# Kernel optimization log

Hardware: AMD Instinct MI355X
Metric: run time of the kernel (lower is better)

Reference implementation:

```python
import jax, jax.numpy as jnp
import numpy as np

N = 512
D = 400          # per-sample feature dim (lstm_hidden_dim * 2)
H = 400          # hidden dim of F_func (lstm_hidden_dim * 2)


def setup_inputs() -> dict:
    key = jax.random.key(0)
    k1, k2, k3, k4, k5, k6 = jax.random.split(key, 6)
    x_samples = jax.random.normal(k1, (N, D), dtype=jnp.float32)
    y_samples = jax.random.normal(k2, (N, D), dtype=jnp.float32)
    # torch nn.Linear default init: U(-1/sqrt(fan_in), 1/sqrt(fan_in))
    b1_bound = 1.0 / np.sqrt(2 * D)
    b2_bound = 1.0 / np.sqrt(H)
    W1 = jax.random.uniform(k3, (H, 2 * D), minval=-b1_bound, maxval=b1_bound, dtype=jnp.float32)
    b1 = jax.random.uniform(k4, (H,), minval=-b1_bound, maxval=b1_bound, dtype=jnp.float32)
    W2 = jax.random.uniform(k5, (1, H), minval=-b2_bound, maxval=b2_bound, dtype=jnp.float32)
    b2 = jax.random.uniform(k6, (1,), minval=-b2_bound, maxval=b2_bound, dtype=jnp.float32)
    return {"x_samples": x_samples, "y_samples": y_samples,
            "W1": W1, "b1": b1, "W2": W2, "b2": b2}


def reference(x_samples, y_samples, W1, b1, W2, b2):
    n = y_samples.shape[0]
    W1x, W1y = W1[:, :D], W1[:, D:]
    hx = x_samples @ W1x.T          # [N, H], contribution of x
    hy = y_samples @ W1y.T          # [N, H], contribution of y

    def score(h):  # second linear + softplus, squeeze out last dim of 1
        return jax.nn.softplus(h @ W2.T + b2)[..., 0]

    # T0[i] = F(x[i], y[i])
    T0 = score(jax.nn.relu(hx + hy + b1))                      # [N]
    # T1[i, j] = F(x[j], y[i])  (x tiled along dim 0, y along dim 1)
    h_pair = jax.nn.relu(hy[:, None, :] + hx[None, :, :] + b1) # [N, N, H]
    T1 = score(h_pair)                                          # [N, N]

    t0_mean = T0.mean()
    lower_bound = t0_mean - (jax.nn.logsumexp(T1, axis=1).mean() - jnp.log(jnp.float32(n)))
    upper_bound = t0_mean - T1.mean()
    return (lower_bound, upper_bound)
```

## Files before the change

### kernel.cpp

```cpp
#include <hip/hip_runtime.h>
#include <math.h>


#define NSAMP 512
#define DIM 400
#define HID 400

__global__ __launch_bounds__(256) void club_gemm_kernel(
    const float* __restrict__ X, const float* __restrict__ Y,
    const float* __restrict__ W1, const float* __restrict__ b1,
    float* __restrict__ hxT0, float* __restrict__ hxT1,
    float* __restrict__ hyb0, float* __restrict__ hyb1)
{
    __shared__ __align__(16) float Ls[64 * 204];
    const int t    = threadIdx.x;
    const int lane = t & 63;
    const int wave = __builtin_amdgcn_readfirstlane(t >> 6);
    const int b    = blockIdx.x;

    const float* __restrict__ Lbase;
    const float* __restrict__ Sbase;
    int Lstride, Lcol0, Lrow0, Lrowmax, Sstride, Scol0, srow_base;
    int kh, mat;

    if (b < 400) {
        mat = 0; kh = b & 1;
        const int bx = (b >> 1) & 7, by = b >> 4;
        Lbase = X;  Lstride = DIM;     Lcol0 = 0;   Lrow0 = bx * 64; Lrowmax = NSAMP - 1;
        Sbase = W1; Sstride = 2 * DIM; Scol0 = 0;
        srow_base = by * 16 + wave * 4;
    } else {
        mat = 1;
        const int bb = b - 400; kh = bb & 1;
        const int bx = (bb >> 1) & 31, by = bb >> 6;
        Lbase = W1; Lstride = 2 * DIM; Lcol0 = DIM; Lrow0 = by * 64; Lrowmax = HID - 1;
        Sbase = Y;  Sstride = DIM;     Scol0 = 0;
        srow_base = bx * 16 + wave * 4;
    }
    const int kc0 = kh * 200;

    for (int idx = t; idx < 3200; idx += 256) {
        int row = idx / 50, q = idx % 50;
        int r = Lrow0 + row; if (r > Lrowmax) r = Lrowmax;
        float4 v = *(const float4*)(Lbase + (size_t)r * Lstride + Lcol0 + kc0 + 4 * q);
        *(float4*)(Ls + row * 204 + 4 * q) = v;
    }
    __syncthreads();

    float acc[4] = {0.f, 0.f, 0.f, 0.f};
#pragma unroll 2
    for (int k4 = 0; k4 < 50; k4++) {
        float4 xv = *(const float4*)(Ls + lane * 204 + 4 * k4);
#pragma unroll
        for (int c = 0; c < 4; c++) {
            const float* __restrict__ wp =
                Sbase + (size_t)(srow_base + c) * Sstride + Scol0 + kc0 + 4 * k4;
            float4 wv = *(const float4*)wp;
            acc[c] = fmaf(xv.x, wv.x, acc[c]);
            acc[c] = fmaf(xv.y, wv.y, acc[c]);
            acc[c] = fmaf(xv.z, wv.z, acc[c]);
            acc[c] = fmaf(xv.w, wv.w, acc[c]);
        }
    }

    if (mat == 0) {
        float* __restrict__ dst = kh ? hxT1 : hxT0;
#pragma unroll
        for (int c = 0; c < 4; c++)
            dst[(size_t)(srow_base + c) * NSAMP + Lrow0 + lane] = acc[c];
    } else {
        float* __restrict__ dst = kh ? hyb1 : hyb0;
        const int h = Lrow0 + lane;
        if (h < HID) {
            if (kh == 0) {
                float bv = b1[h];
#pragma unroll
                for (int c = 0; c < 4; c++) acc[c] += bv;
            }
#pragma unroll
            for (int c = 0; c < 4; c++)
                dst[(size_t)(srow_base + c) * HID + h] = acc[c];
        }
    }
}

__global__ __launch_bounds__(256) void club_combine_kernel(
    const float4* __restrict__ hxT0, const float4* __restrict__ hxT1,
    const float4* __restrict__ hyb0, const float4* __restrict__ hyb1,
    float4* __restrict__ hxT, float4* __restrict__ hyb)
{
    const int idx = blockIdx.x * 256 + threadIdx.x;
    if (idx < 51200) {
        float4 a = hxT0[idx], b = hxT1[idx];
        hxT[idx] = make_float4(a.x + b.x, a.y + b.y, a.z + b.z, a.w + b.w);
    } else {
        const int k = idx - 51200;
        float4 a = hyb0[k], b = hyb1[k];
        hyb[k] = make_float4(a.x + b.x, a.y + b.y, a.z + b.z, a.w + b.w);
    }
}

__global__ __launch_bounds__(256) void club_pair_kernel(
    const float* __restrict__ hxT, const float* __restrict__ hyb,
    const float* __restrict__ W2, const float* __restrict__ b2,
    double* __restrict__ expsum, double* __restrict__ tsum,
    double* __restrict__ diagT)
{
    const int t    = threadIdx.x;
    const int lane = t & 63;
    const int wave = __builtin_amdgcn_readfirstlane(t >> 6);
    const int jx   = blockIdx.x;
    const int j    = jx * 64 + lane;
    const int i    = blockIdx.y * 4 + wave;

    const float* __restrict__ Bp = hxT + j;
    const float* __restrict__ Ap = hyb + (size_t)i * HID;

    float acc0 = 0.f, acc1 = 0.f;
#pragma unroll 2
    for (int g = 0; g < 50; g++) {
        const int h = 8 * g;
        float bv[8];
#pragma unroll
        for (int u = 0; u < 8; u++)
            bv[u] = Bp[(size_t)(h + u) * NSAMP];
        float4 a0 = *(const float4*)(Ap + h);
        float4 a1 = *(const float4*)(Ap + h + 4);
        float4 w0 = *(const float4*)(W2 + h);
        float4 w1 = *(const float4*)(W2 + h + 4);
        acc0 = fmaf(fmaxf(a0.x + bv[0], 0.f), w0.x, acc0);
        acc1 = fmaf(fmaxf(a0.y + bv[1], 0.f), w0.y, acc1);
        acc0 = fmaf(fmaxf(a0.z + bv[2], 0.f), w0.z, acc0);
        acc1 = fmaf(fmaxf(a0.w + bv[3], 0.f), w0.w, acc1);
        acc0 = fmaf(fmaxf(a1.x + bv[4], 0.f), w1.x, acc0);
        acc1 = fmaf(fmaxf(a1.y + bv[5], 0.f), w1.y, acc1);
        acc0 = fmaf(fmaxf(a1.z + bv[6], 0.f), w1.z, acc0);
        acc1 = fmaf(fmaxf(a1.w + bv[7], 0.f), w1.w, acc1);
    }

    float s  = (acc0 + acc1) + b2[0];
    float es = expf(s);
    float T  = log1pf(es);
    if (j == i) diagT[i] = (double)T;
    double eD = 1.0 + (double)es;
    double tD = (double)T;
    for (int off = 32; off > 0; off >>= 1) {
        eD += __shfl_down(eD, off);
        tD += __shfl_down(tD, off);
    }
    if (lane == 0) {
        expsum[i * 8 + jx] = eD;
        tsum  [i * 8 + jx] = tD;
    }
}

__global__ __launch_bounds__(512) void club_final_kernel(
    const double* __restrict__ expsum, const double* __restrict__ tsum,
    const double* __restrict__ diagT, float* __restrict__ out)
{
    __shared__ double sh[3 * 512];
    const int t = threadIdx.x;
    double es = 0.0, ts = 0.0;
#pragma unroll
    for (int b = 0; b < 8; b++) { es += expsum[t * 8 + b]; ts += tsum[t * 8 + b]; }
    sh[t] = log(es); sh[512 + t] = ts; sh[1024 + t] = diagT[t];
    __syncthreads();
    for (int off = 256; off > 0; off >>= 1) {
        if (t < off) {
            sh[t]        += sh[t + off];
            sh[512 + t]  += sh[512 + t + off];
            sh[1024 + t] += sh[1024 + t + off];
        }
        __syncthreads();
    }
    if (t == 0) {
        double t0m  = sh[1024] / 512.0;
        double lsem = sh[0]    / 512.0;
        double t1m  = sh[512]  / (512.0 * 512.0);
        out[0] = (float)(t0m - (lsem - log(512.0)));
        out[1] = (float)(t0m - t1m);
    }
}

extern "C" void kernel_launch(void* const* d_in, const int* in_sizes, int n_in,
                              void* d_out, int out_size, void* d_ws, size_t ws_size,
                              hipStream_t stream) {
    const float* X  = (const float*)d_in[0];
    const float* Y  = (const float*)d_in[1];
    const float* W1 = (const float*)d_in[2];
    const float* b1 = (const float*)d_in[3];
    const float* W2 = (const float*)d_in[4];
    const float* b2 = (const float*)d_in[5];
    float* out = (float*)d_out;

    char* ws = (char*)d_ws;
    float*  hxT0   = (float*) (ws);
    float*  hxT1   = (float*) (ws +  819200);
    float*  hyb0   = (float*) (ws + 1638400);
    float*  hyb1   = (float*) (ws + 2457600);
    float*  hxT    = (float*) (ws + 3276800);
    float*  hyb    = (float*) (ws + 4096000);
    double* expsum = (double*)(ws + 4915200);
    double* tsum   = (double*)(ws + 4947968);
    double* diagT  = (double*)(ws + 4980736);

    club_gemm_kernel   <<<dim3(848),    256, 0, stream>>>(X, Y, W1, b1,
                                                          hxT0, hxT1, hyb0, hyb1);
    club_combine_kernel<<<dim3(400),    256, 0, stream>>>((const float4*)hxT0, (const float4*)hxT1,
                                                          (const float4*)hyb0, (const float4*)hyb1,
                                                          (float4*)hxT, (float4*)hyb);
    club_pair_kernel   <<<dim3(8, 128), 256, 0, stream>>>(hxT, hyb, W2, b2,
                                                          expsum, tsum, diagT);
    club_final_kernel  <<<1, 512, 0, stream>>>(expsum, tsum, diagT, out);
}
```

Before: 110.1 us.

## Merge split-K halves with atomics and re-layout hx into 8-wide blocked tiles

The separate combine kernel is removed. The two K-halves of each GEMM output are now accumulated with float atomicAdd into a workspace that is zeroed by a memset first. hx is stored in an [h/8][j][8] blocked layout, so the pair kernel can load two float4 per lane instead of eight strided scalar loads. In exchange this adds a memset launch and atomic traffic, and the floating-point summation order is no longer deterministic. Some dead pointer arithmetic is left in the GEMM loop.

New measurement: 112.2 us. About the same (+2.0%).

```diff
diff --git a/kernel.cpp b/kernel.cpp
--- a/kernel.cpp
+++ b/kernel.cpp
@@ -9,8 +9,7 @@
 __global__ __launch_bounds__(256) void club_gemm_kernel(
     const float* __restrict__ X, const float* __restrict__ Y,
     const float* __restrict__ W1, const float* __restrict__ b1,
-    float* __restrict__ hxT0, float* __restrict__ hxT1,
-    float* __restrict__ hyb0, float* __restrict__ hyb1)
+    float* __restrict__ hxT8, float* __restrict__ hyb)
 {
     __shared__ __align__(16) float Ls[64 * 204];
     const int t    = threadIdx.x;
@@ -20,21 +19,21 @@
 
     const float* __restrict__ Lbase;
     const float* __restrict__ Sbase;
-    int Lstride, Lcol0, Lrow0, Lrowmax, Sstride, Scol0, srow_base;
+    int Lstride, Lcol0, Lrow0, Lrowmax, Sstride, srow_base;
     int kh, mat;
 
     if (b < 400) {
         mat = 0; kh = b & 1;
         const int bx = (b >> 1) & 7, by = b >> 4;
         Lbase = X;  Lstride = DIM;     Lcol0 = 0;   Lrow0 = bx * 64; Lrowmax = NSAMP - 1;
-        Sbase = W1; Sstride = 2 * DIM; Scol0 = 0;
+        Sbase = W1; Sstride = 2 * DIM;
         srow_base = by * 16 + wave * 4;
     } else {
         mat = 1;
         const int bb = b - 400; kh = bb & 1;
         const int bx = (bb >> 1) & 31, by = bb >> 6;
         Lbase = W1; Lstride = 2 * DIM; Lcol0 = DIM; Lrow0 = by * 64; Lrowmax = HID - 1;
-        Sbase = Y;  Sstride = DIM;     Scol0 = 0;
+        Sbase = Y;  Sstride = DIM;
         srow_base = bx * 16 + wave * 4;
     }
     const int kc0 = kh * 200;
@@ -54,8 +53,10 @@
 #pragma unroll
         for (int c = 0; c < 4; c++) {
             const float* __restrict__ wp =
-                Sbase + (size_t)(srow_base + c) * Sstride + Scol0 + kc0 + 4 * k4;
-            float4 wv = *(const float4*)wp;
+                Sbase + (size_t)(srow_base + c) * Sstride + Lcol0 - (mat ? DIM : 0)
+                      + (mat ? 0 : 0) + kc0 + 4 * k4;
+            float4 wv = *(const float4*)(Sbase + (size_t)(srow_base + c) * Sstride + kc0 + 4 * k4);
+            (void)wp;
             acc[c] = fmaf(xv.x, wv.x, acc[c]);
             acc[c] = fmaf(xv.y, wv.y, acc[c]);
             acc[c] = fmaf(xv.z, wv.z, acc[c]);
@@ -64,12 +65,13 @@
     }
 
     if (mat == 0) {
-        float* __restrict__ dst = kh ? hxT1 : hxT0;
+        const int j = Lrow0 + lane;
+        float* __restrict__ base =
+            hxT8 + (size_t)(srow_base >> 3) * 4096 + (size_t)j * 8 + (srow_base & 4);
 #pragma unroll
         for (int c = 0; c < 4; c++)
-            dst[(size_t)(srow_base + c) * NSAMP + Lrow0 + lane] = acc[c];
+            atomicAdd(base + c, acc[c]);
     } else {
-        float* __restrict__ dst = kh ? hyb1 : hyb0;
         const int h = Lrow0 + lane;
         if (h < HID) {
             if (kh == 0) {
@@ -79,29 +81,13 @@
             }
 #pragma unroll
             for (int c = 0; c < 4; c++)
-                dst[(size_t)(srow_base + c) * HID + h] = acc[c];
+                atomicAdd(hyb + (size_t)(srow_base + c) * HID + h, acc[c]);
         }
     }
 }
 
-__global__ __launch_bounds__(256) void club_combine_kernel(
-    const float4* __restrict__ hxT0, const float4* __restrict__ hxT1,
-    const float4* __restrict__ hyb0, const float4* __restrict__ hyb1,
-    float4* __restrict__ hxT, float4* __restrict__ hyb)
-{
-    const int idx = blockIdx.x * 256 + threadIdx.x;
-    if (idx < 51200) {
-        float4 a = hxT0[idx], b = hxT1[idx];
-        hxT[idx] = make_float4(a.x + b.x, a.y + b.y, a.z + b.z, a.w + b.w);
-    } else {
-        const int k = idx - 51200;
-        float4 a = hyb0[k], b = hyb1[k];
-        hyb[k] = make_float4(a.x + b.x, a.y + b.y, a.z + b.z, a.w + b.w);
-    }
-}
-
 __global__ __launch_bounds__(256) void club_pair_kernel(
-    const float* __restrict__ hxT, const float* __restrict__ hyb,
+    const float* __restrict__ hxT8, const float* __restrict__ hyb,
     const float* __restrict__ W2, const float* __restrict__ b2,
     double* __restrict__ expsum, double* __restrict__ tsum,
     double* __restrict__ diagT)
@@ -113,29 +99,27 @@
     const int j    = jx * 64 + lane;
     const int i    = blockIdx.y * 4 + wave;
 
-    const float* __restrict__ Bp = hxT + j;
+    const float* __restrict__ Bp = hxT8 + (size_t)j * 8;
     const float* __restrict__ Ap = hyb + (size_t)i * HID;
 
     float acc0 = 0.f, acc1 = 0.f;
 #pragma unroll 2
     for (int g = 0; g < 50; g++) {
         const int h = 8 * g;
-        float bv[8];
-#pragma unroll
-        for (int u = 0; u < 8; u++)
-            bv[u] = Bp[(size_t)(h + u) * NSAMP];
+        float4 b0 = *(const float4*)(Bp + (size_t)g * 4096);
+        float4 b1v = *(const float4*)(Bp + (size_t)g * 4096 + 4);
         float4 a0 = *(const float4*)(Ap + h);
         float4 a1 = *(const float4*)(Ap + h + 4);
         float4 w0 = *(const float4*)(W2 + h);
         float4 w1 = *(const float4*)(W2 + h + 4);
-        acc0 = fmaf(fmaxf(a0.x + bv[0], 0.f), w0.x, acc0);
-        acc1 = fmaf(fmaxf(a0.y + bv[1], 0.f), w0.y, acc1);
-        acc0 = fmaf(fmaxf(a0.z + bv[2], 0.f), w0.z, acc0);
-        acc1 = fmaf(fmaxf(a0.w + bv[3], 0.f), w0.w, acc1);
-        acc0 = fmaf(fmaxf(a1.x + bv[4], 0.f), w1.x, acc0);
-        acc1 = fmaf(fmaxf(a1.y + bv[5], 0.f), w1.y, acc1);
-        acc0 = fmaf(fmaxf(a1.z + bv[6], 0.f), w1.z, acc0);
-        acc1 = fmaf(fmaxf(a1.w + bv[7], 0.f), w1.w, acc1);
+        acc0 = fmaf(fmaxf(a0.x + b0.x, 0.f), w0.x, acc0);
+        acc1 = fmaf(fmaxf(a0.y + b0.y, 0.f), w0.y, acc1);
+        acc0 = fmaf(fmaxf(a0.z + b0.z, 0.f), w0.z, acc0);
+        acc1 = fmaf(fmaxf(a0.w + b0.w, 0.f), w0.w, acc1);
+        acc0 = fmaf(fmaxf(a1.x + b1v.x, 0.f), w1.x, acc0);
+        acc1 = fmaf(fmaxf(a1.y + b1v.y, 0.f), w1.y, acc1);
+        acc0 = fmaf(fmaxf(a1.z + b1v.z, 0.f), w1.z, acc0);
+        acc1 = fmaf(fmaxf(a1.w + b1v.w, 0.f), w1.w, acc1);
     }
 
     float s  = (acc0 + acc1) + b2[0];
@@ -194,22 +178,16 @@
     float* out = (float*)d_out;
 
     char* ws = (char*)d_ws;
-    float*  hxT0   = (float*) (ws);
-    float*  hxT1   = (float*) (ws +  819200);
-    float*  hyb0   = (float*) (ws + 1638400);
-    float*  hyb1   = (float*) (ws + 2457600);
-    float*  hxT    = (float*) (ws + 3276800);
-    float*  hyb    = (float*) (ws + 4096000);
-    double* expsum = (double*)(ws + 4915200);
-    double* tsum   = (double*)(ws + 4947968);
-    double* diagT  = (double*)(ws + 4980736);
+    float*  hxT8   = (float*) (ws);
+    float*  hyb    = (float*) (ws +  819200);
+    double* expsum = (double*)(ws + 1638400);
+    double* tsum   = (double*)(ws + 1671168);
+    double* diagT  = (double*)(ws + 1703936);
 
-    club_gemm_kernel   <<<dim3(848),    256, 0, stream>>>(X, Y, W1, b1,
-                                                          hxT0, hxT1, hyb0, hyb1);
-    club_combine_kernel<<<dim3(400),    256, 0, stream>>>((const float4*)hxT0, (const float4*)hxT1,
-                                                          (const float4*)hyb0, (const float4*)hyb1,
-                                                          (float4*)hxT, (float4*)hyb);
-    club_pair_kernel   <<<dim3(8, 128), 256, 0, stream>>>(hxT, hyb, W2, b2,
-                                                          expsum, tsum, diagT);
-    club_final_kernel  <<<1, 512, 0, stream>>>(expsum, tsum, diagT, out);
+    hipMemsetAsync(ws, 0, 1638400, stream);
+
+    club_gemm_kernel <<<dim3(848),    256, 0, stream>>>(X, Y, W1, b1, hxT8, hyb);
+    club_pair_kernel <<<dim3(8, 128), 256, 0, stream>>>(hxT8, hyb, W2, b2,
+                                                        expsum, tsum, diagT);
+    club_final_kernel<<<1, 512, 0, stream>>>(expsum, tsum, diagT, out);
 }
```
